# Optimization experiments

Measured on AMD Instinct MI355X. Metric: run time of the kernel, lower is better.

Reference implementation:

```python
import jax, jax.numpy as jnp
import numpy as np
from jax import lax

# config (matches init_kwargs)
HEADS = 4
KD2 = 256          # key_dim // 2
KNN = 16
BLOCK = 128        # knn * block_rate
COL = 512          # value_size // block
VALUE_SIZE = 65536 # key_num ** 2
D_OUT = 512
D_IN = 1024
QUERYDIM = HEADS * KD2  # 1024
KERNEL = 3


def setup_inputs() -> dict:
    key = jax.random.key(0)
    ks = jax.random.split(key, 8)
    B, T = 2, 2048
    return {
        "x": jax.random.normal(ks[0], (B, T, D_IN), dtype=jnp.float32),
        "conv_w": jax.random.normal(ks[1], (D_IN, 1, KERNEL), dtype=jnp.float32) * 0.1,
        "conv_b": jax.random.normal(ks[2], (D_IN,), dtype=jnp.float32) * 0.1,
        "lin_w": jax.random.normal(ks[3], (QUERYDIM, D_IN), dtype=jnp.float32) * (D_IN ** -0.5),
        "lin_b": jax.random.normal(ks[4], (QUERYDIM,), dtype=jnp.float32) * 0.1,
        "rowkeys": jax.random.normal(ks[5], (BLOCK, HEADS, KD2), dtype=jnp.float32) * (KD2 ** -0.5),
        "colkeys": jax.random.normal(ks[6], (COL, HEADS, KD2), dtype=jnp.float32) * (KD2 ** -0.5),
        "value_w": jax.random.normal(ks[7], (VALUE_SIZE, D_OUT), dtype=jnp.float32),
    }


def _forward(x, conv_w, conv_b, lin_w, lin_b, rowkeys, colkeys, value_w):
    B, T, C = x.shape
    # --- Querynet: causal depthwise conv1d + linear ---
    xt = jnp.transpose(x, (0, 2, 1))  # (B, C, T)
    y = lax.conv_general_dilated(
        xt, conv_w, window_strides=(1,), padding=[(KERNEL - 1, 0)],
        feature_group_count=C, dimension_numbers=("NCH", "OIH", "NCH"))
    y = y + conv_b[None, :, None]
    y = jnp.transpose(y, (0, 2, 1))                     # (B, T, C)
    query = y @ lin_w.T + lin_b                         # (B, T, querydim)
    # torch: query.view(B, heads, T, key_dim//2) -- raw C-order reshape
    q = query.reshape(B, HEADS, T, KD2)
    # --- block_wise_choice.get_indices ---
    score = jnp.einsum("bhtd,ehd->bhte", q, rowkeys)    # (B,H,T,block)
    col_scores = jnp.einsum("bhtd,chd->bhtc", q, colkeys)  # (B,H,T,col)
    score_col, idx_col = lax.top_k(col_scores, 1)       # (B,H,T,1)
    base = jnp.arange(BLOCK, dtype=jnp.int32)
    indices = base[None, None, None, :] * COL + idx_col  # (B,H,T,block)
    score = score + score_col                            # broadcast add
    # torch .view(B,H,-1,T): raw C-order reshape mixing tokens and blocks
    score = score.reshape(B, HEADS, BLOCK, T)
    indices = indices.reshape(B, HEADS, BLOCK, T)
    k = T * KNN // BLOCK
    score_top, dispatch = lax.top_k(score, k)            # (B,H,block,k), sorted desc
    idx_top = jnp.take_along_axis(indices, dispatch, axis=-1)
    score_r = score_top.reshape(B, BLOCK, -1)            # (B, block, H*k)
    idx_r = idx_top.reshape(B, BLOCK, -1)
    disp_r = dispatch.reshape(B, BLOCK, -1)
    # --- Memory_value: gather-weight-scatter ---
    gathered = value_w[idx_r]                            # (B, block, H*k, d)
    weighted = (gathered * score_r[..., None]).reshape(B, -1, D_OUT)
    flat_disp = disp_r.reshape(B, -1)                    # values in [0, T)
    out = jnp.zeros((B, T, D_OUT), dtype=weighted.dtype)
    out = out.at[jnp.arange(B)[:, None], flat_disp].add(weighted)
    return out


def reference(x, conv_w, conv_b, lin_w, lin_b, rowkeys, colkeys, value_w):
    return _forward(x, conv_w, conv_b, lin_w, lin_b, rowkeys, colkeys, value_w)
```

## Files before the change

### kernel.cpp

```cpp
#include <hip/hip_runtime.h>

constexpr int Bc   = 2;
constexpr int Tc   = 2048;
constexpr int Cc   = 1024;
constexpr int QDc  = 1024;
constexpr int Hc   = 4;
constexpr int KD2c = 256;
constexpr int BLKc = 128;
constexpr int COLc = 512;
constexpr int DOUTc= 512;
constexpr int KSELc= 256;
constexpr int NKEYS= BLKc + COLc;
constexpr int NBINS= Bc * Tc;
constexpr int NSEL = Bc * Hc * BLKc * KSELc;

typedef short bf16x8 __attribute__((ext_vector_type(8)));
typedef float f32x4  __attribute__((ext_vector_type(4)));

__device__ __forceinline__ unsigned short f2bf(float f) {
    unsigned u = __float_as_uint(f);
    u += 0x7FFFu + ((u >> 16) & 1u);
    return (unsigned short)(u >> 16);
}
__device__ __forceinline__ float bf2f(unsigned short h) {
    return __uint_as_float((unsigned)h << 16);
}
__device__ __forceinline__ void splitbf3(float f, unsigned short* h,
                                         unsigned short* m, unsigned short* l) {
    unsigned short hh = f2bf(f);
    float r1 = f - bf2f(hh);
    unsigned short mm = f2bf(r1);
    float r2 = r1 - bf2f(mm);
    *h = hh; *m = mm; *l = f2bf(r2);
}

__device__ __forceinline__ void gld_lds16(const void* g, void* l) {
    __builtin_amdgcn_global_load_lds(
        (const __attribute__((address_space(1))) unsigned int*)g,
        (__attribute__((address_space(3))) unsigned int*)l, 16, 0, 0);
}

__global__ __launch_bounds__(256) void conv_kernel(
    const float* __restrict__ x, const float* __restrict__ cw,
    const float* __restrict__ cb, unsigned short* __restrict__ y1,
    unsigned short* __restrict__ y2, unsigned short* __restrict__ y3)
{
    int idx = blockIdx.x * 256 + threadIdx.x;
    int c = idx & (Cc - 1);
    int t = (idx >> 10) & (Tc - 1);
    int b = idx >> 21;
    float w0 = cw[c*3+0], w1 = cw[c*3+1], w2 = cw[c*3+2];
    const float* xb = x + (size_t)b * Tc * Cc;
    float acc = cb[c] + w2 * xb[(size_t)t*Cc + c];
    if (t >= 1) acc += w1 * xb[(size_t)(t-1)*Cc + c];
    if (t >= 2) acc += w0 * xb[(size_t)(t-2)*Cc + c];
    splitbf3(acc, &y1[idx], &y2[idx], &y3[idx]);
}

__global__ __launch_bounds__(256) void convw_kernel(
    const float* __restrict__ w, unsigned short* __restrict__ w1,
    unsigned short* __restrict__ w2, unsigned short* __restrict__ w3)
{
    int idx = blockIdx.x * 256 + threadIdx.x;
    splitbf3(w[idx], &w1[idx], &w2[idx], &w3[idx]);
}

__global__ __launch_bounds__(256) void convkeys_kernel(
    const float* __restrict__ rowkeys, const float* __restrict__ colkeys,
    unsigned short* __restrict__ k1, unsigned short* __restrict__ k2,
    unsigned short* __restrict__ k3)
{
    int bid = blockIdx.x;
    int h = bid / NKEYS, n = bid % NKEYS;
    int k = threadIdx.x;
    float v = (n < BLKc) ? rowkeys[((size_t)n*Hc + h)*KD2c + k]
                         : colkeys[((size_t)(n-BLKc)*Hc + h)*KD2c + k];
    size_t o = ((size_t)h*NKEYS + n)*KD2c + k;
    splitbf3(v, &k1[o], &k2[o], &k3[o]);
}

__device__ __forceinline__ void mfma_gemm_tile(
    const unsigned short* __restrict__ A1g, const unsigned short* __restrict__ A2g,
    const unsigned short* __restrict__ A3g, int lda,
    const unsigned short* __restrict__ B1g, const unsigned short* __restrict__ B2g,
    const unsigned short* __restrict__ B3g, int ldb,
    int K, int m0, int n0, char* lds, f32x4 acc[4][2])
{
    const int tid  = threadIdx.x;
    const int wave = tid >> 6, lane = tid & 63;
    const int wr = wave >> 2, wc = wave & 3;
    const int g = lane >> 4, r16 = lane & 15;

    int aoff[4], boff[2];
    #pragma unroll
    for (int i = 0; i < 4; i++) {
        int ra = wr*64 + i*16 + r16;
        aoff[i] = ra*64 + ((g ^ ((ra>>1)&3)) << 4);
    }
    #pragma unroll
    for (int j = 0; j < 2; j++) {
        int rb = wc*32 + j*16 + r16;
        boff[j] = rb*64 + ((g ^ ((rb>>1)&3)) << 4);
    }
    const int row0 = tid >> 2, kg0 = ((tid & 3) ^ ((row0>>1)&3)) * 8;
    char* d0 = lds + wave*1024;

#define STAGE(kc, bo) do {                                                 \
        size_t a0_ = (size_t)(m0+row0)*lda + (kc) + kg0;                   \
        size_t b0_ = (size_t)(n0+row0)*ldb + (kc) + kg0;                   \
        gld_lds16(A1g + a0_, d0 + (bo));                                   \
        gld_lds16(A2g + a0_, d0 + 8192 + (bo));                            \
        gld_lds16(A3g + a0_, d0 + 16384 + (bo));                           \
        gld_lds16(B1g + b0_, d0 + 24576 + (bo));                           \
        gld_lds16(B2g + b0_, d0 + 32768 + (bo));                           \
        gld_lds16(B3g + b0_, d0 + 40960 + (bo));                           \
    } while (0)

    auto compute = [&](int bo) {
        bf16x8 a1[4], a2[4], a3[4], b1[2], b2[2], b3[2];
        #pragma unroll
        for (int i = 0; i < 4; i++) {
            a1[i] = *(const bf16x8*)(lds + bo + aoff[i]);
            a2[i] = *(const bf16x8*)(lds + bo +  8192 + aoff[i]);
            a3[i] = *(const bf16x8*)(lds + bo + 16384 + aoff[i]);
        }
        #pragma unroll
        for (int j = 0; j < 2; j++) {
            b1[j] = *(const bf16x8*)(lds + bo + 24576 + boff[j]);
            b2[j] = *(const bf16x8*)(lds + bo + 32768 + boff[j]);
            b3[j] = *(const bf16x8*)(lds + bo + 40960 + boff[j]);
        }
        #pragma unroll
        for (int i = 0; i < 4; i++)
            #pragma unroll
            for (int j = 0; j < 2; j++) {
                acc[i][j] = __builtin_amdgcn_mfma_f32_16x16x32_bf16(a3[i], b1[j], acc[i][j], 0, 0, 0);
                acc[i][j] = __builtin_amdgcn_mfma_f32_16x16x32_bf16(a2[i], b2[j], acc[i][j], 0, 0, 0);
                acc[i][j] = __builtin_amdgcn_mfma_f32_16x16x32_bf16(a1[i], b3[j], acc[i][j], 0, 0, 0);
                acc[i][j] = __builtin_amdgcn_mfma_f32_16x16x32_bf16(a2[i], b1[j], acc[i][j], 0, 0, 0);
                acc[i][j] = __builtin_amdgcn_mfma_f32_16x16x32_bf16(a1[i], b2[j], acc[i][j], 0, 0, 0);
                acc[i][j] = __builtin_amdgcn_mfma_f32_16x16x32_bf16(a1[i], b1[j], acc[i][j], 0, 0, 0);
            }
    };

    const int NT = K / 32;
    STAGE(0, 0);
    int bo = 0;
    for (int t = 0; t < NT - 1; ++t) {
        STAGE((t+1)*32, bo ^ 49152);
        asm volatile("s_waitcnt vmcnt(6)" ::: "memory");
        __builtin_amdgcn_s_barrier();
        asm volatile("" ::: "memory");
        compute(bo);
        asm volatile("" ::: "memory");
        __builtin_amdgcn_s_barrier();
        bo ^= 49152;
    }
    asm volatile("s_waitcnt vmcnt(0)" ::: "memory");
    __builtin_amdgcn_s_barrier();
    asm volatile("" ::: "memory");
    compute(bo);
#undef STAGE
}

__global__ __launch_bounds__(512) void qgemm_kernel(
    const unsigned short* __restrict__ y1, const unsigned short* __restrict__ y2,
    const unsigned short* __restrict__ y3,
    const unsigned short* __restrict__ w1, const unsigned short* __restrict__ w2,
    const unsigned short* __restrict__ w3,
    const float* __restrict__ bias,
    unsigned short* __restrict__ q1, unsigned short* __restrict__ q2,
    unsigned short* __restrict__ q3)
{
    __shared__ char lds[98304];
    int m0 = blockIdx.y * 128, n0 = blockIdx.x * 128;
    f32x4 acc[4][2];
    #pragma unroll
    for (int i = 0; i < 4; i++)
        #pragma unroll
        for (int j = 0; j < 2; j++) acc[i][j] = (f32x4)0.f;
    mfma_gemm_tile(y1, y2, y3, Cc, w1, w2, w3, Cc, Cc, m0, n0, lds, acc);

    const int lane = threadIdx.x & 63, wave = threadIdx.x >> 6;
    const int wr = wave >> 2, wc = wave & 3;
    const int g = lane >> 4, r16 = lane & 15;
    #pragma unroll
    for (int i = 0; i < 4; i++)
        #pragma unroll
        for (int j = 0; j < 2; j++)
            #pragma unroll
            for (int reg = 0; reg < 4; reg++) {
                int m = m0 + wr*64 + i*16 + g*4 + reg;
                int n = n0 + wc*32 + j*16 + r16;
                float v = acc[i][j][reg] + bias[n];
                size_t o = (size_t)m * QDc + n;
                splitbf3(v, &q1[o], &q2[o], &q3[o]);
            }
}

__global__ __launch_bounds__(512) void sgemm_kernel(
    const unsigned short* __restrict__ q1, const unsigned short* __restrict__ q2,
    const unsigned short* __restrict__ q3,
    const unsigned short* __restrict__ k1, const unsigned short* __restrict__ k2,
    const unsigned short* __restrict__ k3,
    float* __restrict__ Ctmp)
{
    __shared__ char lds[98304];
    int b4h = blockIdx.z;
    size_t qo = (size_t)b4h * (Tc * KD2c);
    size_t ko = (size_t)(b4h & 3) * (NKEYS * KD2c);
    int m0 = blockIdx.y * 128, n0 = blockIdx.x * 128;
    f32x4 acc[4][2];
    #pragma unroll
    for (int i = 0; i < 4; i++)
        #pragma unroll
        for (int j = 0; j < 2; j++) acc[i][j] = (f32x4)0.f;
    mfma_gemm_tile(q1+qo, q2+qo, q3+qo, KD2c, k1+ko, k2+ko, k3+ko, KD2c,
                   KD2c, m0, n0, lds, acc);

    const int lane = threadIdx.x & 63, wave = threadIdx.x >> 6;
    const int wr = wave >> 2, wc = wave & 3;
    const int g = lane >> 4, r16 = lane & 15;
    float* Cb = Ctmp + (size_t)b4h * Tc * NKEYS;
    #pragma unroll
    for (int i = 0; i < 4; i++)
        #pragma unroll
        for (int j = 0; j < 2; j++)
            #pragma unroll
            for (int reg = 0; reg < 4; reg++) {
                int m = m0 + wr*64 + i*16 + g*4 + reg;
                int n = n0 + wc*32 + j*16 + r16;
                Cb[(size_t)m * NKEYS + n] = acc[i][j][reg];
            }
}

__global__ __launch_bounds__(256) void colmax_kernel(
    const float* __restrict__ Ctmp, float* __restrict__ s, int* __restrict__ cidx)
{
    int rid = blockIdx.x * 4 + (threadIdx.x >> 6);
    int lane = threadIdx.x & 63;
    const float* row = Ctmp + (size_t)rid * NKEYS;
    float best = -3.4e38f; int bi = 0;
    #pragma unroll
    for (int i = 0; i < 8; i++) {
        int c = lane + i*64;
        float v = row[BLKc + c];
        if (v > best) { best = v; bi = c; }
    }
    #pragma unroll
    for (int off = 32; off > 0; off >>= 1) {
        float ov = __shfl_xor(best, off, 64);
        int   oi = __shfl_xor(bi,   off, 64);
        if (ov > best || (ov == best && oi < bi)) { best = ov; bi = oi; }
    }
    if (lane == 0) cidx[rid] = bi;
    #pragma unroll
    for (int e = lane; e < BLKc; e += 64)
        s[(size_t)rid*BLKc + e] = row[e] + best;
}

__global__ __launch_bounds__(256) void topk_kernel(
    const float* __restrict__ s, const int* __restrict__ cidx,
    int* __restrict__ tk_j, int* __restrict__ tk_vidx, float* __restrict__ tk_score)
{
    int wid  = (blockIdx.x << 2) + (threadIdx.x >> 6);
    int lane = threadIdx.x & 63;
    int batch = wid >> 7;
    int i = wid & 127;
    const float* srow = s + (size_t)batch * (Tc*BLKc) + (size_t)i * 2048;

    unsigned key[8][4];
    #pragma unroll
    for (int r = 0; r < 8; r++) {
        float4 v4 = *(const float4*)&srow[r*256 + lane*4];
        float vv[4] = {v4.x, v4.y, v4.z, v4.w};
        #pragma unroll
        for (int e = 0; e < 4; e++) {
            unsigned u = __float_as_uint(vv[e]);
            key[r][e] = (u >> 31) ? ~u : (u | 0x80000000u);
        }
    }

    unsigned lo = 0, hi = 0xFFFFFFFFu;
    while (lo < hi) {
        unsigned d = hi - lo;
        unsigned mid = lo + ((d >> 1) + (d & 1u));
        int cnt = 0;
        #pragma unroll
        for (int r = 0; r < 8; r++)
            #pragma unroll
            for (int e = 0; e < 4; e++)
                cnt += (key[r][e] >= mid) ? 1 : 0;
        #pragma unroll
        for (int off = 32; off > 0; off >>= 1) cnt += __shfl_xor(cnt, off, 64);
        if (cnt >= KSELc) lo = mid; else hi = mid - 1;
    }
    const unsigned thr = lo;

    int gcnt = 0, ecnt = 0;
    unsigned eqmask = 0;
    #pragma unroll
    for (int r = 0; r < 8; r++)
        #pragma unroll
        for (int e = 0; e < 4; e++) {
            gcnt += (key[r][e] > thr) ? 1 : 0;
            if (key[r][e] == thr) { eqmask |= (1u << (r*4+e)); ecnt++; }
        }

    int gpre = gcnt, epre = ecnt;
    #pragma unroll
    for (int off = 1; off < 64; off <<= 1) {
        int gv = __shfl_up(gpre, off, 64);
        int ev = __shfl_up(epre, off, 64);
        if (lane >= off) { gpre += gv; epre += ev; }
    }
    const int total_greater = __shfl(gpre, 63, 64);
    const int total_eq      = __shfl(epre, 63, 64);
    const int gbase = gpre - gcnt;
    const int ebase = epre - ecnt;
    const int need  = KSELc - total_greater;

    const size_t obase = (size_t)wid * KSELc;
    const int cbase = batch * Tc + i * 16;

    int rk = 0;
    #pragma unroll
    for (int r = 0; r < 8; r++)
        #pragma unroll
        for (int e = 0; e < 4; e++) {
            if (key[r][e] > thr) {
                int j = r*256 + lane*4 + e;
                unsigned u = key[r][e];
                float f = (u >> 31) ? __uint_as_float(u ^ 0x80000000u)
                                    : __uint_as_float(~u);
                size_t o = obase + gbase + rk;
                tk_j[o] = j;
                tk_vidx[o] = (j & 127) * COLc + cidx[cbase + (j >> 7)];
                tk_score[o] = f;
                rk++;
            }
        }

    if (need == total_eq) {
        int erk = 0;
        #pragma unroll
        for (int r = 0; r < 8; r++)
            #pragma unroll
            for (int e = 0; e < 4; e++) {
                if (key[r][e] == thr) {
                    int j = r*256 + lane*4 + e;
                    float f = (thr >> 31) ? __uint_as_float(thr ^ 0x80000000u)
                                          : __uint_as_float(~thr);
                    size_t o = obase + total_greater + ebase + erk;
                    tk_j[o] = j;
                    tk_vidx[o] = (j & 127) * COLc + cidx[cbase + (j >> 7)];
                    tk_score[o] = f;
                    erk++;
                }
            }
    } else {
        unsigned em = eqmask;
        int left = need;
        while (left > 0) {
            int myj = 0x7FFFFFFF;
            if (em) {
                int bit = __builtin_ctz(em);
                myj = (bit >> 2)*256 + lane*4 + (bit & 3);
            }
            int mn = myj;
            #pragma unroll
            for (int off = 32; off > 0; off >>= 1) mn = min(mn, __shfl_xor(mn, off, 64));
            if (myj == mn) {
                em &= em - 1;
                int j = mn;
                float f = (thr >> 31) ? __uint_as_float(thr ^ 0x80000000u)
                                      : __uint_as_float(~thr);
                size_t o = obase + (KSELc - left);
                tk_j[o] = j;
                tk_vidx[o] = (j & 127) * COLc + cidx[cbase + (j >> 7)];
                tk_score[o] = f;
            }
            left--;
        }
    }
}

__global__ __launch_bounds__(256) void zero_bins_kernel(int* __restrict__ p, int n)
{
    int i = blockIdx.x * 256 + threadIdx.x;
    if (i < n) p[i] = 0;
}

__global__ __launch_bounds__(256) void count_kernel(
    const int* __restrict__ tk_j, int* __restrict__ counts)
{
    int idx = blockIdx.x * 256 + threadIdx.x;
    int r = idx >> 8;
    int b = r >> 9;
    int j = tk_j[idx];
    atomicAdd(&counts[b * Tc + j], 1);
}

__global__ __launch_bounds__(256) void scan_kernel(
    const int* __restrict__ counts, int* __restrict__ offsets)
{
    __shared__ int part[256];
    int tid = threadIdx.x;
    int local[16];
    int sum = 0;
    #pragma unroll
    for (int k = 0; k < 16; k++) { local[k] = sum; sum += counts[tid*16 + k]; }
    part[tid] = sum;
    __syncthreads();
    for (int st = 1; st < 256; st <<= 1) {
        int v = (tid >= st) ? part[tid - st] : 0;
        __syncthreads();
        part[tid] += v;
        __syncthreads();
    }
    int base = (tid == 0) ? 0 : part[tid - 1];
    #pragma unroll
    for (int k = 0; k < 16; k++) offsets[tid*16 + k] = base + local[k];
    if (tid == 255) offsets[NBINS] = base + sum;
}

__global__ __launch_bounds__(256) void fill_kernel(
    const int* __restrict__ tk_j, const int* __restrict__ tk_vidx,
    const float* __restrict__ tk_score, const int* __restrict__ offsets,
    int* __restrict__ fillctr, int* __restrict__ bin_vidx,
    float* __restrict__ bin_score)
{
    int idx = blockIdx.x * 256 + threadIdx.x;
    int r = idx >> 8;
    int b = r >> 9;
    int bin = b * Tc + tk_j[idx];
    int pos = offsets[bin] + atomicAdd(&fillctr[bin], 1);
    bin_vidx[pos]  = tk_vidx[idx];
    bin_score[pos] = tk_score[idx];
}

__global__ __launch_bounds__(256) void gather_kernel(
    const int* __restrict__ offsets, const int* __restrict__ bin_vidx,
    const float* __restrict__ bin_score, const float* __restrict__ value_w,
    float* __restrict__ out)
{
    __shared__ int   svidx[512];
    __shared__ float sscore[512];
    int bin = blockIdx.x;
    int tid = threadIdx.x;
    int beg = offsets[bin], cnt = offsets[bin + 1] - beg;
    for (int n = tid; n < cnt; n += 256) {
        svidx[n]  = bin_vidx[beg + n];
        sscore[n] = bin_score[beg + n];
    }
    __syncthreads();

    const int c = tid * 2;
    float accx = 0.f, accy = 0.f;
    int n = 0;
    for (; n + 8 <= cnt; n += 8) {
        int vi[8]; float sc[8]; float2 vv[8];
        #pragma unroll
        for (int k = 0; k < 8; k++) { vi[k] = svidx[n+k]; sc[k] = sscore[n+k]; }
        #pragma unroll
        for (int k = 0; k < 8; k++)
            vv[k] = *(const float2*)&value_w[(size_t)vi[k] * DOUTc + c];
        #pragma unroll
        for (int k = 0; k < 8; k++) { accx += sc[k]*vv[k].x; accy += sc[k]*vv[k].y; }
    }
    for (; n < cnt; n++) {
        int v = svidx[n]; float sc = sscore[n];
        float2 a = *(const float2*)&value_w[(size_t)v * DOUTc + c];
        accx += sc*a.x; accy += sc*a.y;
    }
    float2 res; res.x = accx; res.y = accy;
    *(float2*)&out[(size_t)bin * DOUTc + c] = res;
}

extern "C" void kernel_launch(void* const* d_in, const int* in_sizes, int n_in,
                              void* d_out, int out_size, void* d_ws, size_t ws_size,
                              hipStream_t stream)
{
    const float* x       = (const float*)d_in[0];
    const float* conv_w  = (const float*)d_in[1];
    const float* conv_b  = (const float*)d_in[2];
    const float* lin_w   = (const float*)d_in[3];
    const float* lin_b   = (const float*)d_in[4];
    const float* rowkeys = (const float*)d_in[5];
    const float* colkeys = (const float*)d_in[6];
    const float* value_w = (const float*)d_in[7];
    float* out = (float*)d_out;

    constexpr size_t MB = 1024*1024;
    char* w = (char*)d_ws;
    float*          Ctmp = (float*)(w);
    unsigned short* y1   = (unsigned short*)(w);
    unsigned short* y2   = (unsigned short*)(w +  8*MB);
    unsigned short* y3   = (unsigned short*)(w + 16*MB);
    unsigned short* w1   = (unsigned short*)(w + 24*MB);
    unsigned short* w2   = (unsigned short*)(w + 26*MB);
    unsigned short* w3   = (unsigned short*)(w + 28*MB);
    unsigned short* q1   = (unsigned short*)(w + 40*MB);
    unsigned short* q2   = (unsigned short*)(w + 48*MB);
    unsigned short* q3   = (unsigned short*)(w + 56*MB);
    unsigned short* k1   = (unsigned short*)(w + 64*MB);
    unsigned short* k2   = (unsigned short*)(w + 66*MB);
    unsigned short* k3   = (unsigned short*)(w + 68*MB);
    float*          s    = (float*)(w + 70*MB);
    int*            cidx = (int*)  (w + 78*MB);
    int*            tk_j = (int*)  (w + 79*MB);
    int*            tk_v = (int*)  (w + 80*MB);
    float*          tk_s = (float*)(w + 81*MB);
    int*            counts    = (int*)  (w + 82*MB);
    int*            offsets   = (int*)  (w + 82*MB + 32768);
    int*            fillctr   = (int*)  (w + 82*MB + 65536);
    int*            bin_vidx  = (int*)  (w + 82*MB + 131072);
    float*          bin_score = (float*)(w + 82*MB + 131072 + 1048576);

    conv_kernel<<<(Bc*Tc*Cc)/256, 256, 0, stream>>>(x, conv_w, conv_b, y1, y2, y3);
    convw_kernel<<<(QDc*Cc)/256, 256, 0, stream>>>(lin_w, w1, w2, w3);
    convkeys_kernel<<<Hc*NKEYS, 256, 0, stream>>>(rowkeys, colkeys, k1, k2, k3);
    qgemm_kernel<<<dim3(QDc/128, (Bc*Tc)/128), 512, 0, stream>>>(
        y1, y2, y3, w1, w2, w3, lin_b, q1, q2, q3);
    sgemm_kernel<<<dim3(NKEYS/128, Tc/128, Bc*Hc), 512, 0, stream>>>(
        q1, q2, q3, k1, k2, k3, Ctmp);
    colmax_kernel<<<(Bc*Hc*Tc)/4, 256, 0, stream>>>(Ctmp, s, cidx);
    topk_kernel<<<Bc*Hc*BLKc/4, 256, 0, stream>>>(s, cidx, tk_j, tk_v, tk_s);
    zero_bins_kernel<<<(96*1024/4 + 255)/256, 256, 0, stream>>>(counts, 96*1024/4);
    count_kernel<<<NSEL/256, 256, 0, stream>>>(tk_j, counts);
    scan_kernel<<<1, 256, 0, stream>>>(counts, offsets);
    fill_kernel<<<NSEL/256, 256, 0, stream>>>(tk_j, tk_v, tk_s, offsets,
                                              fillctr, bin_vidx, bin_score);
    gather_kernel<<<NBINS, 256, 0, stream>>>(offsets, bin_vidx, bin_score,
                                             value_w, out);
}
```

Baseline: 237.3 us.

## Split output bins into 64-entry chunks for load-balanced gather with atomic merge

Replaces the one-block-per-output-row gather with a chunk list. Each row's entries are split into chunks of up to 64, and each chunk is gathered by a 128-thread block that loads float4 values. Rows with several chunks combine their results with atomicAdd, so the output is now zeroed up front. This is meant to balance load across rows with skewed counts and to widen memory accesses, at the cost of extra kernels, atomics, and a nondeterministic summation order.

After: 261.0 us. 10.0% more time.

```diff
diff --git a/kernel.cpp b/kernel.cpp
--- a/kernel.cpp
+++ b/kernel.cpp
@@ -13,6 +13,7 @@
 constexpr int NKEYS= BLKc + COLc;
 constexpr int NBINS= Bc * Tc;
 constexpr int NSEL = Bc * Hc * BLKc * KSELc;
+constexpr int MAXCHUNKS = 8192;
 
 typedef short bf16x8 __attribute__((ext_vector_type(8)));
 typedef float f32x4  __attribute__((ext_vector_type(4)));
@@ -391,6 +392,12 @@
     if (i < n) p[i] = 0;
 }
 
+__global__ __launch_bounds__(256) void zero_out_kernel(float4* __restrict__ p, int n4)
+{
+    int i = blockIdx.x * 256 + threadIdx.x;
+    if (i < n4) p[i] = float4{0.f, 0.f, 0.f, 0.f};
+}
+
 __global__ __launch_bounds__(256) void count_kernel(
     const int* __restrict__ tk_j, int* __restrict__ counts)
 {
@@ -439,42 +446,69 @@
     bin_score[pos] = tk_score[idx];
 }
 
-__global__ __launch_bounds__(256) void gather_kernel(
-    const int* __restrict__ offsets, const int* __restrict__ bin_vidx,
-    const float* __restrict__ bin_score, const float* __restrict__ value_w,
-    float* __restrict__ out)
-{
-    __shared__ int   svidx[512];
-    __shared__ float sscore[512];
-    int bin = blockIdx.x;
-    int tid = threadIdx.x;
-    int beg = offsets[bin], cnt = offsets[bin + 1] - beg;
-    for (int n = tid; n < cnt; n += 256) {
-        svidx[n]  = bin_vidx[beg + n];
-        sscore[n] = bin_score[beg + n];
-    }
+__global__ __launch_bounds__(256) void chunks_kernel(
+    const int* __restrict__ offsets, int* __restrict__ nchunks,
+    int4* __restrict__ chunks)
+{
+    int bin = blockIdx.x * 256 + threadIdx.x;
+    if (bin >= NBINS) return;
+    int beg = offsets[bin], end = offsets[bin + 1];
+    int cnt = end - beg;
+    if (cnt <= 0) return;
+    int nch = (cnt + 63) >> 6;
+    int base = atomicAdd(nchunks, nch);
+    for (int k = 0; k < nch; k++) {
+        int cb = beg + k * 64;
+        int ce = min(end, cb + 64);
+        chunks[base + k] = make_int4(bin, cb, ce, (nch > 1) ? 1 : 0);
+    }
+}
+
+__global__ __launch_bounds__(128) void gather_kernel(
+    const int* __restrict__ nchunks, const int4* __restrict__ chunks,
+    const int* __restrict__ bin_vidx, const float* __restrict__ bin_score,
+    const float* __restrict__ value_w, float* __restrict__ out)
+{
+    if ((int)blockIdx.x >= *nchunks) return;
+    int4 ch = chunks[blockIdx.x];
+    const int bin = ch.x, beg = ch.y, cnt = ch.z - ch.y, multi = ch.w;
+    const int tid = threadIdx.x;
+
+    __shared__ int   svidx[64];
+    __shared__ float sscore[64];
+    if (tid < cnt) { svidx[tid] = bin_vidx[beg + tid]; sscore[tid] = bin_score[beg + tid]; }
     __syncthreads();
 
-    const int c = tid * 2;
-    float accx = 0.f, accy = 0.f;
+    const int c = tid * 4;
+    float4 acc = {0.f, 0.f, 0.f, 0.f};
     int n = 0;
     for (; n + 8 <= cnt; n += 8) {
-        int vi[8]; float sc[8]; float2 vv[8];
+        int vi[8]; float sc[8]; float4 vv[8];
         #pragma unroll
         for (int k = 0; k < 8; k++) { vi[k] = svidx[n+k]; sc[k] = sscore[n+k]; }
         #pragma unroll
         for (int k = 0; k < 8; k++)
-            vv[k] = *(const float2*)&value_w[(size_t)vi[k] * DOUTc + c];
-        #pragma unroll
-        for (int k = 0; k < 8; k++) { accx += sc[k]*vv[k].x; accy += sc[k]*vv[k].y; }
+            vv[k] = *(const float4*)&value_w[(size_t)vi[k] * DOUTc + c];
+        #pragma unroll
+        for (int k = 0; k < 8; k++) {
+            acc.x += sc[k]*vv[k].x; acc.y += sc[k]*vv[k].y;
+            acc.z += sc[k]*vv[k].z; acc.w += sc[k]*vv[k].w;
+        }
     }
     for (; n < cnt; n++) {
         int v = svidx[n]; float sc = sscore[n];
-        float2 a = *(const float2*)&value_w[(size_t)v * DOUTc + c];
-        accx += sc*a.x; accy += sc*a.y;
-    }
-    float2 res; res.x = accx; res.y = accy;
-    *(float2*)&out[(size_t)bin * DOUTc + c] = res;
+        float4 a = *(const float4*)&value_w[(size_t)v * DOUTc + c];
+        acc.x += sc*a.x; acc.y += sc*a.y; acc.z += sc*a.z; acc.w += sc*a.w;
+    }
+    float* orow = out + (size_t)bin * DOUTc + c;
+    if (multi) {
+        atomicAdd(&orow[0], acc.x);
+        atomicAdd(&orow[1], acc.y);
+        atomicAdd(&orow[2], acc.z);
+        atomicAdd(&orow[3], acc.w);
+    } else {
+        *(float4*)orow = acc;
+    }
 }
 
 extern "C" void kernel_launch(void* const* d_in, const int* in_sizes, int n_in,
@@ -514,8 +548,10 @@
     int*            counts    = (int*)  (w + 82*MB);
     int*            offsets   = (int*)  (w + 82*MB + 32768);
     int*            fillctr   = (int*)  (w + 82*MB + 65536);
+    int*            nchunks   = (int*)  (w + 82*MB + 81920);
     int*            bin_vidx  = (int*)  (w + 82*MB + 131072);
     float*          bin_score = (float*)(w + 82*MB + 131072 + 1048576);
+    int4*           chunks    = (int4*) (w + 82*MB + 131072 + 2097152);
 
     conv_kernel<<<(Bc*Tc*Cc)/256, 256, 0, stream>>>(x, conv_w, conv_b, y1, y2, y3);
     convw_kernel<<<(QDc*Cc)/256, 256, 0, stream>>>(lin_w, w1, w2, w3);
@@ -527,10 +563,12 @@
     colmax_kernel<<<(Bc*Hc*Tc)/4, 256, 0, stream>>>(Ctmp, s, cidx);
     topk_kernel<<<Bc*Hc*BLKc/4, 256, 0, stream>>>(s, cidx, tk_j, tk_v, tk_s);
     zero_bins_kernel<<<(96*1024/4 + 255)/256, 256, 0, stream>>>(counts, 96*1024/4);
+    zero_out_kernel<<<(out_size/4 + 255)/256, 256, 0, stream>>>((float4*)out, out_size/4);
     count_kernel<<<NSEL/256, 256, 0, stream>>>(tk_j, counts);
     scan_kernel<<<1, 256, 0, stream>>>(counts, offsets);
     fill_kernel<<<NSEL/256, 256, 0, stream>>>(tk_j, tk_v, tk_s, offsets,
                                               fillctr, bin_vidx, bin_score);
-    gather_kernel<<<NBINS, 256, 0, stream>>>(offsets, bin_vidx, bin_score,
-                                             value_w, out);
-}
+    chunks_kernel<<<(NBINS + 255)/256, 256, 0, stream>>>(offsets, nchunks, chunks);
+    gather_kernel<<<MAXCHUNKS, 128, 0, stream>>>(nchunks, chunks, bin_vidx,
+                                                 bin_score, value_w, out);
+}
```
